# Optimization experiments

Hardware: AMD Instinct MI355X
Metric: run time of the kernel (lower is better)

The kernel has to match this reference:

```python
import jax, jax.numpy as jnp
import numpy as np

B, L, N = 16, 512, 5
D_WORD, HID = 200, 768
LN_EPS = 1e-12
INIT_STD = 0.02


def setup_inputs() -> dict:
    key = jax.random.key(0)
    ks = jax.random.split(key, 10)
    layer_output = jax.random.normal(ks[0], (B, L, HID), dtype=jnp.float32)
    word_embeddings = jax.random.normal(ks[1], (B, L, N, D_WORD), dtype=jnp.float32)
    word_mask = jax.random.randint(ks[2], (B, L, N), 0, 2, dtype=jnp.int32)
    # linear layers: torch nn.Linear init ~ U(-1/sqrt(fan_in), 1/sqrt(fan_in))
    w1_bound = 1.0 / np.sqrt(D_WORD)
    w2_bound = 1.0 / np.sqrt(HID)
    W1 = jax.random.uniform(ks[3], (D_WORD, HID), jnp.float32, -w1_bound, w1_bound)
    b1 = jax.random.uniform(ks[4], (HID,), jnp.float32, -w1_bound, w1_bound)
    W2 = jax.random.uniform(ks[5], (HID, HID), jnp.float32, -w2_bound, w2_bound)
    b2 = jax.random.uniform(ks[6], (HID,), jnp.float32, -w2_bound, w2_bound)
    attn_W = jax.random.normal(ks[7], (HID, HID), dtype=jnp.float32) * INIT_STD
    gamma = jnp.ones((HID,), dtype=jnp.float32)
    beta = jnp.zeros((HID,), dtype=jnp.float32)
    return {
        "layer_output": layer_output,
        "word_embeddings": word_embeddings,
        "word_mask": word_mask,
        "W1": W1, "b1": b1, "W2": W2, "b2": b2,
        "attn_W": attn_W, "gamma": gamma, "beta": beta,
    }


def reference(layer_output, word_embeddings, word_mask, W1, b1, W2, b2, attn_W, gamma, beta):
    # MLP over word embeddings: [B,L,N,D_word] -> [B,L,N,HID]
    word_outputs = jnp.tanh(word_embeddings @ W1 + b1) @ W2 + b2
    # dropout is identity in eval mode
    # bilinear attention scores: (layer_output @ attn_W) . word_outputs -> [B,L,N]
    scores = jnp.einsum('bld,de,blne->bln', layer_output, attn_W, word_outputs)
    scores = jnp.where(word_mask != 0, jnp.float32(-1e9), scores)
    attn = jax.nn.softmax(scores, axis=-1)  # [B,L,N]
    weighted = jnp.einsum('bln,blnh->blh', attn, word_outputs)
    out = layer_output + weighted
    # LayerNorm over last dim
    mu = jnp.mean(out, axis=-1, keepdims=True)
    var = jnp.mean(jnp.square(out - mu), axis=-1, keepdims=True)
    out = (out - mu) * jax.lax.rsqrt(var + LN_EPS) * gamma + beta
    return out
```

## Files before the change

kernel.cpp:

```cpp
#include <hip/hip_runtime.h>
#include <hip/hip_bf16.h>

#define HID 768
#define DW  200
#define NW  5


__device__ __forceinline__ float fast_tanh(float x) {
    float ax = fabsf(x);
    float z  = __expf(-2.0f * ax);
    float r  = (1.0f - z) * __builtin_amdgcn_rcpf(1.0f + z);
    return copysignf(r, x);
}

__global__ __launch_bounds__(256)
void gw_kernel(const float* __restrict__ A,
               const float* __restrict__ W2,
               float* __restrict__ G)
{
    __shared__ __align__(16) float AsT[32][68];
    __shared__ __align__(16) float WsT[32][68];
    const int tid = threadIdx.x;
    const int bd = blockIdx.x / (HID / 64), bh = blockIdx.x % (HID / 64);
    const int d0 = bd * 64, h0 = bh * 64;
    const int tx = tid % 16, ty = tid / 16;

    float acc[4][4];
    #pragma unroll
    for (int i = 0; i < 4; ++i)
        #pragma unroll
        for (int j = 0; j < 4; ++j) acc[i][j] = 0.f;

    for (int e0 = 0; e0 < HID; e0 += 32) {
        __syncthreads();
        #pragma unroll
        for (int q = 0; q < 2; ++q) {
            int idx = q * 256 + tid;
            int r = idx / 8, c4 = idx % 8;
            float4 va = *reinterpret_cast<const float4*>(&A [(size_t)(d0 + r) * HID + e0 + c4 * 4]);
            AsT[c4 * 4 + 0][r] = va.x; AsT[c4 * 4 + 1][r] = va.y;
            AsT[c4 * 4 + 2][r] = va.z; AsT[c4 * 4 + 3][r] = va.w;
            float4 vw = *reinterpret_cast<const float4*>(&W2[(size_t)(h0 + r) * HID + e0 + c4 * 4]);
            WsT[c4 * 4 + 0][r] = vw.x; WsT[c4 * 4 + 1][r] = vw.y;
            WsT[c4 * 4 + 2][r] = vw.z; WsT[c4 * 4 + 3][r] = vw.w;
        }
        __syncthreads();
        #pragma unroll 4
        for (int e = 0; e < 32; ++e) {
            float4 a4 = *reinterpret_cast<const float4*>(&AsT[e][ty * 4]);
            float4 b4 = *reinterpret_cast<const float4*>(&WsT[e][tx * 4]);
            float av[4] = {a4.x, a4.y, a4.z, a4.w};
            float bv[4] = {b4.x, b4.y, b4.z, b4.w};
            #pragma unroll
            for (int i = 0; i < 4; ++i)
                #pragma unroll
                for (int j = 0; j < 4; ++j)
                    acc[i][j] = fmaf(av[i], bv[j], acc[i][j]);
        }
    }
    #pragma unroll
    for (int i = 0; i < 4; ++i) {
        float4 o = {acc[i][0], acc[i][1], acc[i][2], acc[i][3]};
        *reinterpret_cast<float4*>(&G[(size_t)(d0 + ty * 4 + i) * HID + h0 + tx * 4]) = o;
    }
}

template<int TT>
__global__ __launch_bounds__(256)
void proj_kernel(const float* __restrict__ LO,
                 const float* __restrict__ G,
                 float* __restrict__ P2)
{
    __shared__ __align__(16) float loT[HID][TT];
    const int tid = threadIdx.x;
    const long tok0 = (long)blockIdx.x * TT;

    {
        const float4* src = reinterpret_cast<const float4*>(LO + tok0 * HID);
        for (int i = tid; i < TT * (HID / 4); i += 256) {
            int t = i / (HID / 4), k4 = i % (HID / 4);
            float4 v = src[(size_t)t * (HID / 4) + k4];
            loT[k4 * 4 + 0][t] = v.x; loT[k4 * 4 + 1][t] = v.y;
            loT[k4 * 4 + 2][t] = v.z; loT[k4 * 4 + 3][t] = v.w;
        }
    }
    __syncthreads();

    float acc[TT][3];
    #pragma unroll
    for (int t = 0; t < TT; ++t) { acc[t][0] = 0.f; acc[t][1] = 0.f; acc[t][2] = 0.f; }

    #pragma unroll 2
    for (int k = 0; k < HID; ++k) {
        float a[TT];
        #pragma unroll
        for (int q = 0; q < TT / 4; ++q) {
            float4 v = *reinterpret_cast<const float4*>(&loT[k][q * 4]);
            a[q * 4 + 0] = v.x; a[q * 4 + 1] = v.y; a[q * 4 + 2] = v.z; a[q * 4 + 3] = v.w;
        }
        float w0 = G[(size_t)k * HID + tid];
        float w1 = G[(size_t)k * HID + 256 + tid];
        float w2 = G[(size_t)k * HID + 512 + tid];
        #pragma unroll
        for (int t = 0; t < TT; ++t) {
            acc[t][0] = fmaf(a[t], w0, acc[t][0]);
            acc[t][1] = fmaf(a[t], w1, acc[t][1]);
            acc[t][2] = fmaf(a[t], w2, acc[t][2]);
        }
    }

    #pragma unroll
    for (int c = 0; c < 3; ++c)
        #pragma unroll
        for (int t = 0; t < TT; ++t)
            P2[(tok0 + t) * HID + c * 256 + tid] = acc[t][c];
}

#define KSPLIT 100

__global__ __launch_bounds__(256, 4)
void fused_kernel(const float* __restrict__ WE,
                  const float* __restrict__ W1,
                  const float* __restrict__ b1,
                  const float* __restrict__ W2,
                  const float* __restrict__ b2,
                  const float* __restrict__ LO,
                  const float* __restrict__ P2,
                  const int* __restrict__ mask,
                  const float* __restrict__ gamma,
                  const float* __restrict__ beta,
                  float* __restrict__ out)
{
    __shared__ __align__(16) float smem[HID * 4];
    __shared__ float red[4][32];
    __shared__ float sc_s[4][NW];
    __shared__ float at_s[4][NW];
    __shared__ float mus[4], rss[4];

    const int tid = threadIdx.x;
    const int wave = tid >> 6, lane = tid & 63;
    const long tok0 = (long)blockIdx.x * 4;
    const long row0 = tok0 * NW;

    float p2v[4][3];
    #pragma unroll
    for (int tt = 0; tt < 4; ++tt) {
        p2v[tt][0] = P2[(tok0 + tt) * HID + tid];
        p2v[tt][1] = P2[(tok0 + tt) * HID + 256 + tid];
        p2v[tt][2] = P2[(tok0 + tt) * HID + 512 + tid];
    }

    float th[20][3];
    #pragma unroll
    for (int r = 0; r < 20; ++r) { th[r][0] = 0.f; th[r][1] = 0.f; th[r][2] = 0.f; }

    #pragma unroll 1
    for (int half = 0; half < 2; ++half) {
        const int kbase = half * KSPLIT;
        __syncthreads();
        for (int i = tid; i < 20 * (KSPLIT / 4); i += 256) {
            int r = i / (KSPLIT / 4), k4 = i % (KSPLIT / 4);
            float4 v = *reinterpret_cast<const float4*>(&WE[(row0 + r) * DW + kbase + k4 * 4]);
            smem[(k4 * 4 + 0) * 20 + r] = v.x;
            smem[(k4 * 4 + 1) * 20 + r] = v.y;
            smem[(k4 * 4 + 2) * 20 + r] = v.z;
            smem[(k4 * 4 + 3) * 20 + r] = v.w;
        }
        __syncthreads();

        #pragma unroll 2
        for (int kk = 0; kk < KSPLIT; ++kk) {
            int k = kbase + kk;
            float a[20];
            #pragma unroll
            for (int q = 0; q < 5; ++q) {
                float4 v = *reinterpret_cast<const float4*>(&smem[kk * 20 + q * 4]);
                a[q * 4 + 0] = v.x; a[q * 4 + 1] = v.y; a[q * 4 + 2] = v.z; a[q * 4 + 3] = v.w;
            }
            float w0 = W1[(size_t)k * HID + tid];
            float w1 = W1[(size_t)k * HID + 256 + tid];
            float w2 = W1[(size_t)k * HID + 512 + tid];
            #pragma unroll
            for (int r = 0; r < 20; ++r) {
                th[r][0] = fmaf(a[r], w0, th[r][0]);
                th[r][1] = fmaf(a[r], w1, th[r][1]);
                th[r][2] = fmaf(a[r], w2, th[r][2]);
            }
        }
    }
    {
        float bb0 = b1[tid], bb1 = b1[256 + tid], bb2 = b1[512 + tid];
        #pragma unroll
        for (int r = 0; r < 20; ++r) {
            th[r][0] = fast_tanh(th[r][0] + bb0);
            th[r][1] = fast_tanh(th[r][1] + bb1);
            th[r][2] = fast_tanh(th[r][2] + bb2);
        }
    }

    #pragma unroll
    for (int tt = 0; tt < 4; ++tt)
        #pragma unroll
        for (int n = 0; n < NW; ++n) {
            int r = tt * NW + n;
            float s = th[r][0] * p2v[tt][0];
            s = fmaf(th[r][1], p2v[tt][1], s);
            s = fmaf(th[r][2], p2v[tt][2], s);
            #pragma unroll
            for (int off = 32; off; off >>= 1) s += __shfl_xor(s, off);
            if (lane == 0) red[wave][r] = s;
        }
    __syncthreads();
    if (tid < 20) {
        float s = red[0][tid] + red[1][tid] + red[2][tid] + red[3][tid];
        sc_s[tid / NW][tid % NW] = s;
    }
    __syncthreads();

    if (tid < 4) {
        float v[NW]; float m = -3.0e38f;
        #pragma unroll
        for (int n = 0; n < NW; ++n) {
            float sv = (mask[(tok0 + tid) * NW + n] != 0) ? -1.0e9f : sc_s[tid][n];
            v[n] = sv; m = fmaxf(m, sv);
        }
        float sum = 0.f;
        #pragma unroll
        for (int n = 0; n < NW; ++n) { float e = expf(v[n] - m); v[n] = e; sum += e; }
        float inv = 1.0f / sum;
        #pragma unroll
        for (int n = 0; n < NW; ++n) at_s[tid][n] = v[n] * inv;
    }
    __syncthreads();

    #pragma unroll
    for (int tt = 0; tt < 4; ++tt) {
        float a0 = 0.f, a1 = 0.f, a2 = 0.f;
        #pragma unroll
        for (int n = 0; n < NW; ++n) {
            float w = at_s[tt][n];
            a0 = fmaf(w, th[tt * NW + n][0], a0);
            a1 = fmaf(w, th[tt * NW + n][1], a1);
            a2 = fmaf(w, th[tt * NW + n][2], a2);
        }
        smem[(0 * 256 + tid) * 4 + tt] = a0;
        smem[(1 * 256 + tid) * 4 + tt] = a1;
        smem[(2 * 256 + tid) * 4 + tt] = a2;
    }
    __syncthreads();

    float acc[4][3];
    #pragma unroll
    for (int t = 0; t < 4; ++t) { acc[t][0] = 0.f; acc[t][1] = 0.f; acc[t][2] = 0.f; }

    #pragma unroll 4
    for (int k = 0; k < HID; ++k) {
        float4 a4 = *reinterpret_cast<const float4*>(&smem[k * 4]);
        float w0 = W2[(size_t)k * HID + tid];
        float w1 = W2[(size_t)k * HID + 256 + tid];
        float w2 = W2[(size_t)k * HID + 512 + tid];
        acc[0][0] = fmaf(a4.x, w0, acc[0][0]); acc[0][1] = fmaf(a4.x, w1, acc[0][1]); acc[0][2] = fmaf(a4.x, w2, acc[0][2]);
        acc[1][0] = fmaf(a4.y, w0, acc[1][0]); acc[1][1] = fmaf(a4.y, w1, acc[1][1]); acc[1][2] = fmaf(a4.y, w2, acc[1][2]);
        acc[2][0] = fmaf(a4.z, w0, acc[2][0]); acc[2][1] = fmaf(a4.z, w1, acc[2][1]); acc[2][2] = fmaf(a4.z, w2, acc[2][2]);
        acc[3][0] = fmaf(a4.w, w0, acc[3][0]); acc[3][1] = fmaf(a4.w, w1, acc[3][1]); acc[3][2] = fmaf(a4.w, w2, acc[3][2]);
    }

    float v[4][3];
    {
        float bb0 = b2[tid], bb1 = b2[256 + tid], bb2 = b2[512 + tid];
        #pragma unroll
        for (int t = 0; t < 4; ++t) {
            v[t][0] = acc[t][0] + bb0 + LO[(tok0 + t) * HID + tid];
            v[t][1] = acc[t][1] + bb1 + LO[(tok0 + t) * HID + 256 + tid];
            v[t][2] = acc[t][2] + bb2 + LO[(tok0 + t) * HID + 512 + tid];
        }
    }

    #pragma unroll
    for (int t = 0; t < 4; ++t) {
        float s = v[t][0] + v[t][1] + v[t][2];
        float q = v[t][0] * v[t][0];
        q = fmaf(v[t][1], v[t][1], q);
        q = fmaf(v[t][2], v[t][2], q);
        #pragma unroll
        for (int off = 32; off; off >>= 1) { s += __shfl_xor(s, off); q += __shfl_xor(q, off); }
        if (lane == 0) { red[wave][t] = s; red[wave][4 + t] = q; }
    }
    __syncthreads();
    if (tid < 4) {
        float S = red[0][tid] + red[1][tid] + red[2][tid] + red[3][tid];
        float Q = red[0][4 + tid] + red[1][4 + tid] + red[2][4 + tid] + red[3][4 + tid];
        float mu = S * (1.0f / HID);
        float var = Q * (1.0f / HID) - mu * mu;
        mus[tid] = mu;
        rss[tid] = rsqrtf(var + 1e-12f);
    }
    __syncthreads();

    {
        float g0 = gamma[tid], g1 = gamma[256 + tid], g2 = gamma[512 + tid];
        float e0 = beta[tid],  e1 = beta[256 + tid],  e2 = beta[512 + tid];
        #pragma unroll
        for (int t = 0; t < 4; ++t) {
            float mu = mus[t], rs = rss[t];
            out[(tok0 + t) * HID + tid]       = (v[t][0] - mu) * rs * g0 + e0;
            out[(tok0 + t) * HID + 256 + tid] = (v[t][1] - mu) * rs * g1 + e1;
            out[(tok0 + t) * HID + 512 + tid] = (v[t][2] - mu) * rs * g2 + e2;
        }
    }
}

extern "C" void kernel_launch(void* const* d_in, const int* in_sizes, int n_in,
                              void* d_out, int out_size, void* d_ws, size_t ws_size,
                              hipStream_t stream)
{
    const float* LO    = (const float*)d_in[0];
    const float* WE    = (const float*)d_in[1];
    const int*   mask  = (const int*)  d_in[2];
    const float* W1    = (const float*)d_in[3];
    const float* b1    = (const float*)d_in[4];
    const float* W2    = (const float*)d_in[5];
    const float* b2    = (const float*)d_in[6];
    const float* attnW = (const float*)d_in[7];
    const float* gamma = (const float*)d_in[8];
    const float* beta  = (const float*)d_in[9];
    float* out = (float*)d_out;

    const int T = 16 * 512;

    float* P2 = (float*)d_ws;
    float* G  = P2 + (size_t)T * HID;

    gw_kernel<<<(HID / 64) * (HID / 64), 256, 0, stream>>>(attnW, W2, G);
    proj_kernel<8><<<T / 8, 256, 0, stream>>>(LO, G, P2);
    fused_kernel<<<T / 4, 256, 0, stream>>>(WE, W1, b1, W2, b2, LO, P2, mask, gamma, beta, out);
}
```

Measured before the change: 693.7 us.

## Fuse layer-output projection into main kernel, removing separate proj kernel and P2 buffer

```diff
diff --git a/kernel.cpp b/kernel.cpp
--- a/kernel.cpp
+++ b/kernel.cpp
@@ -65,67 +65,16 @@
     }
 }
 
-template<int TT>
-__global__ __launch_bounds__(256)
-void proj_kernel(const float* __restrict__ LO,
-                 const float* __restrict__ G,
-                 float* __restrict__ P2)
-{
-    __shared__ __align__(16) float loT[HID][TT];
-    const int tid = threadIdx.x;
-    const long tok0 = (long)blockIdx.x * TT;
-
-    {
-        const float4* src = reinterpret_cast<const float4*>(LO + tok0 * HID);
-        for (int i = tid; i < TT * (HID / 4); i += 256) {
-            int t = i / (HID / 4), k4 = i % (HID / 4);
-            float4 v = src[(size_t)t * (HID / 4) + k4];
-            loT[k4 * 4 + 0][t] = v.x; loT[k4 * 4 + 1][t] = v.y;
-            loT[k4 * 4 + 2][t] = v.z; loT[k4 * 4 + 3][t] = v.w;
-        }
-    }
-    __syncthreads();
-
-    float acc[TT][3];
-    #pragma unroll
-    for (int t = 0; t < TT; ++t) { acc[t][0] = 0.f; acc[t][1] = 0.f; acc[t][2] = 0.f; }
-
-    #pragma unroll 2
-    for (int k = 0; k < HID; ++k) {
-        float a[TT];
-        #pragma unroll
-        for (int q = 0; q < TT / 4; ++q) {
-            float4 v = *reinterpret_cast<const float4*>(&loT[k][q * 4]);
-            a[q * 4 + 0] = v.x; a[q * 4 + 1] = v.y; a[q * 4 + 2] = v.z; a[q * 4 + 3] = v.w;
-        }
-        float w0 = G[(size_t)k * HID + tid];
-        float w1 = G[(size_t)k * HID + 256 + tid];
-        float w2 = G[(size_t)k * HID + 512 + tid];
-        #pragma unroll
-        for (int t = 0; t < TT; ++t) {
-            acc[t][0] = fmaf(a[t], w0, acc[t][0]);
-            acc[t][1] = fmaf(a[t], w1, acc[t][1]);
-            acc[t][2] = fmaf(a[t], w2, acc[t][2]);
-        }
-    }
-
-    #pragma unroll
-    for (int c = 0; c < 3; ++c)
-        #pragma unroll
-        for (int t = 0; t < TT; ++t)
-            P2[(tok0 + t) * HID + c * 256 + tid] = acc[t][c];
-}
-
 #define KSPLIT 100
 
-__global__ __launch_bounds__(256, 4)
+__global__
 void fused_kernel(const float* __restrict__ WE,
                   const float* __restrict__ W1,
                   const float* __restrict__ b1,
                   const float* __restrict__ W2,
                   const float* __restrict__ b2,
                   const float* __restrict__ LO,
-                  const float* __restrict__ P2,
+                  const float* __restrict__ G,
                   const int* __restrict__ mask,
                   const float* __restrict__ gamma,
                   const float* __restrict__ beta,
@@ -142,12 +91,30 @@
     const long tok0 = (long)blockIdx.x * 4;
     const long row0 = tok0 * NW;
 
+    for (int i = tid; i < 4 * (HID / 4); i += 256) {
+        int t = i / (HID / 4), k4 = i % (HID / 4);
+        float4 v = *reinterpret_cast<const float4*>(&LO[(tok0 + t) * HID + k4 * 4]);
+        smem[(k4 * 4 + 0) * 4 + t] = v.x;
+        smem[(k4 * 4 + 1) * 4 + t] = v.y;
+        smem[(k4 * 4 + 2) * 4 + t] = v.z;
+        smem[(k4 * 4 + 3) * 4 + t] = v.w;
+    }
+    __syncthreads();
+
     float p2v[4][3];
     #pragma unroll
-    for (int tt = 0; tt < 4; ++tt) {
-        p2v[tt][0] = P2[(tok0 + tt) * HID + tid];
-        p2v[tt][1] = P2[(tok0 + tt) * HID + 256 + tid];
-        p2v[tt][2] = P2[(tok0 + tt) * HID + 512 + tid];
+    for (int tt = 0; tt < 4; ++tt) { p2v[tt][0] = 0.f; p2v[tt][1] = 0.f; p2v[tt][2] = 0.f; }
+
+    #pragma unroll 4
+    for (int k = 0; k < HID; ++k) {
+        float4 a4 = *reinterpret_cast<const float4*>(&smem[k * 4]);
+        float g0 = G[(size_t)k * HID + tid];
+        float g1 = G[(size_t)k * HID + 256 + tid];
+        float g2 = G[(size_t)k * HID + 512 + tid];
+        p2v[0][0] = fmaf(a4.x, g0, p2v[0][0]); p2v[0][1] = fmaf(a4.x, g1, p2v[0][1]); p2v[0][2] = fmaf(a4.x, g2, p2v[0][2]);
+        p2v[1][0] = fmaf(a4.y, g0, p2v[1][0]); p2v[1][1] = fmaf(a4.y, g1, p2v[1][1]); p2v[1][2] = fmaf(a4.y, g2, p2v[1][2]);
+        p2v[2][0] = fmaf(a4.z, g0, p2v[2][0]); p2v[2][1] = fmaf(a4.z, g1, p2v[2][1]); p2v[2][2] = fmaf(a4.z, g2, p2v[2][2]);
+        p2v[3][0] = fmaf(a4.w, g0, p2v[3][0]); p2v[3][1] = fmaf(a4.w, g1, p2v[3][1]); p2v[3][2] = fmaf(a4.w, g2, p2v[3][2]);
     }
 
     float th[20][3];
@@ -328,10 +295,8 @@
 
     const int T = 16 * 512;
 
-    float* P2 = (float*)d_ws;
-    float* G  = P2 + (size_t)T * HID;
+    float* G = (float*)d_ws;
 
     gw_kernel<<<(HID / 64) * (HID / 64), 256, 0, stream>>>(attnW, W2, G);
-    proj_kernel<8><<<T / 8, 256, 0, stream>>>(LO, G, P2);
-    fused_kernel<<<T / 4, 256, 0, stream>>>(WE, W1, b1, W2, b2, LO, P2, mask, gamma, beta, out);
+    fused_kernel<<<T / 4, 256, 0, stream>>>(WE, W1, b1, W2, b2, LO, G, mask, gamma, beta, out);
 }
```

Result: slower. 737.8 us (+6.4%).
